# Optimization experiments

Measured on AMD Instinct MI355X. Metric: run time of the kernel, lower is better.

Reference implementation:

```python
import jax, jax.numpy as jnp
import numpy as np

B, S, D, H, L, NITEMS = 512, 200, 64, 2, 2, 100000
HD = D // H
EPS = 1e-8
C = 0.001


def _ln(x, w, b):
    m = jnp.mean(x, -1, keepdims=True)
    v = jnp.mean((x - m) ** 2, -1, keepdims=True)
    return (x - m) / jnp.sqrt(v + EPS) * w + b


def _frob(x):
    return jnp.sqrt(jnp.sum(x * x))


def setup_inputs() -> dict:
    key = jax.random.key(0)
    ks = jax.random.split(key, 20)
    rn = lambda k, shape, s=0.02: jax.random.normal(k, shape, jnp.float32) * s
    item_emb = rn(ks[0], (NITEMS + 1, D))
    pos_emb = rn(ks[1], (S + 1, D)).at[0].set(0.0)  # padding_idx=0 row
    pred_w = rn(ks[2], (1, D))
    inp = {
        'user_ids': jax.random.randint(ks[3], (B,), 0, NITEMS, dtype=jnp.int32),
        'log_seqs': jax.random.randint(ks[4], (B, S), 0, NITEMS + 1, dtype=jnp.int32),
        'pos_seqs': jax.random.randint(ks[5], (B, S), 0, NITEMS + 1, dtype=jnp.int32),
        'item_emb': item_emb, 'pos_emb': pos_emb, 'pred_w': pred_w,
        'ln_w': jnp.ones((L, D), jnp.float32), 'ln_b': rn(ks[6], (L, D)),
        'qkv_w': rn(ks[7], (L, 3 * D, D)), 'qkv_b': rn(ks[8], (L, 3 * D)),
        'out_w': rn(ks[9], (L, D, D)), 'out_b': rn(ks[10], (L, D)),
        'fc1_w': rn(ks[11], (L, D, D)), 'fc1_b': rn(ks[12], (L, D)),
        'ffln_w': jnp.ones((L, D), jnp.float32), 'ffln_b': rn(ks[13], (L, D)),
        'fc2_w': rn(ks[14], (L, D, D)), 'fc2_b': rn(ks[15], (L, D)),
        'ffln2_w': jnp.ones((L, D), jnp.float32), 'ffln2_b': rn(ks[16], (L, D)),
    }
    return inp


def reference(user_ids, log_seqs, pos_seqs, item_emb, pos_emb, pred_w,
              ln_w, ln_b, qkv_w, qkv_b, out_w, out_b,
              fc1_w, fc1_b, ffln_w, ffln_b, fc2_w, fc2_b, ffln2_w, ffln2_b):
    # ---- log2feats ----
    x = item_emb[log_seqs] * jnp.sqrt(jnp.float32(D))  # (B,S,D)
    poss = jnp.arange(1, S + 1, dtype=log_seqs.dtype)[None, :] * (log_seqs != 0)
    x = x + pos_emb[poss]
    causal_bias = jnp.where(jnp.tril(jnp.ones((S, S), bool)), 0.0, -1e30).astype(jnp.float32)
    for l in range(L):
        q_in = _ln(x, ln_w[l], ln_b[l])  # query uses pre-LN, K/V use raw seqs
        q = (q_in @ qkv_w[l, :D].T + qkv_b[l, :D]).reshape(B, S, H, HD)
        k = (x @ qkv_w[l, D:2 * D].T + qkv_b[l, D:2 * D]).reshape(B, S, H, HD)
        v = (x @ qkv_w[l, 2 * D:].T + qkv_b[l, 2 * D:]).reshape(B, S, H, HD)
        sc = jnp.einsum('bqhd,bkhd->bhqk', q, k) / jnp.sqrt(jnp.float32(HD)) + causal_bias
        a = jax.nn.softmax(sc, -1)
        ctx = jnp.einsum('bhqk,bkhd->bqhd', a, v).reshape(B, S, D)
        x = q_in + ctx @ out_w[l].T + out_b[l]
        h = jax.nn.relu(_ln(x, ffln_w[l], ffln_b[l]) @ fc1_w[l].T + fc1_b[l])
        x = h @ fc2_w[l].T + fc2_b[l] + _ln(x, ffln2_w[l], ffln2_b[l])
    # ---- left(): quadratic form via Gram matrices (math identical to outer-product sum) ----
    FF = jnp.einsum('bsi,bsj->ij', x, x)          # sum_b F_b^T F_b  (d,d)
    EE = item_emb.T @ item_emb                      # (d,d)
    hh = pred_w.T @ pred_w                          # (d,d)
    left = C * jnp.sum(FF * EE * hh)
    # ---- right() ----
    ps = (x * item_emb[pos_seqs]) @ pred_w[0]       # (B,S), prediction has no bias
    right = jnp.sum((1.0 - C) * ps ** 2 - 2.0 * ps)
    # ---- reg_loss(): sum of per-parameter Frobenius norms ----
    reg = _frob(item_emb) + _frob(pos_emb) + _frob(pred_w)
    for p in (ln_w, ln_b, qkv_w, qkv_b, out_w, out_b, fc1_w, fc1_b,
              ffln_w, ffln_b, fc2_w, fc2_b, ffln2_w, ffln2_b):
        reg = reg + jnp.sum(jax.vmap(_frob)(p))  # per-layer params are separate tensors
    return left + right + 0.1 * reg
```

## Files before the change

### kernel.cpp

```cpp
#include <hip/hip_runtime.h>
#include <math.h>

#define BB 512
#define SS 200
#define DDIM 64
#define HD 32
#define LL 2
#define NROWS (BB * SS)
#define EPS 1e-8f
#define CC 0.001f
#define GRAM_NB 256
#define LSTRIDE 72
#define XS 68
#define QROWS 208

typedef __attribute__((ext_vector_type(8))) short bf16x8;
typedef __attribute__((ext_vector_type(4))) float f32x4;

__device__ unsigned short g_qb[NROWS * DDIM];
__device__ float g_gpart[2 * GRAM_NB * 4096];

__device__ __forceinline__ float wave_sum(float v) {
#pragma unroll
    for (int o = 32; o > 0; o >>= 1) v += __shfl_xor(v, o, 64);
    return v;
}
__device__ __forceinline__ unsigned short f2b(float f) {
    unsigned u = __float_as_uint(f);
    return (unsigned short)((u + 0x7FFFu + ((u >> 16) & 1u)) >> 16);
}

__device__ __forceinline__ bf16x8 frag_raw(const float* Xf, int row, int c0) {
    const float* p = &Xf[row * XS + c0];
    float4 u = *(const float4*)p;
    float4 v = *(const float4*)(p + 4);
    bf16x8 r;
    r[0] = (short)f2b(u.x); r[1] = (short)f2b(u.y); r[2] = (short)f2b(u.z); r[3] = (short)f2b(u.w);
    r[4] = (short)f2b(v.x); r[5] = (short)f2b(v.y); r[6] = (short)f2b(v.z); r[7] = (short)f2b(v.w);
    return r;
}
__device__ __forceinline__ bf16x8 frag_ln(const float* Xf, const float* stats,
                                          const float* vw, const float* vb,
                                          int row, int c0) {
    float m = stats[row * 2], rs = stats[row * 2 + 1];
    const float* p = &Xf[row * XS + c0];
    float4 u = *(const float4*)p;
    float4 v = *(const float4*)(p + 4);
    bf16x8 r;
    r[0] = (short)f2b((u.x - m) * rs * vw[c0 + 0] + vb[c0 + 0]);
    r[1] = (short)f2b((u.y - m) * rs * vw[c0 + 1] + vb[c0 + 1]);
    r[2] = (short)f2b((u.z - m) * rs * vw[c0 + 2] + vb[c0 + 2]);
    r[3] = (short)f2b((u.w - m) * rs * vw[c0 + 3] + vb[c0 + 3]);
    r[4] = (short)f2b((v.x - m) * rs * vw[c0 + 4] + vb[c0 + 4]);
    r[5] = (short)f2b((v.y - m) * rs * vw[c0 + 5] + vb[c0 + 5]);
    r[6] = (short)f2b((v.z - m) * rs * vw[c0 + 6] + vb[c0 + 6]);
    r[7] = (short)f2b((v.w - m) * rs * vw[c0 + 7] + vb[c0 + 7]);
    return r;
}

__device__ __forceinline__ void stage_wf32(const float* __restrict__ G,
                                           unsigned short* __restrict__ L, int t) {
    int r = t >> 4, c4 = (t & 15) * 4;
    float4 f = *(const float4*)&G[r * 64 + c4];
    ushort4 o; o.x = f2b(f.x); o.y = f2b(f.y); o.z = f2b(f.z); o.w = f2b(f.w);
    *(ushort4*)&L[r * LSTRIDE + c4] = o;
}

__global__ __launch_bounds__(1024)
void mega(const int* __restrict__ log_seqs,
          const int* __restrict__ pos_seqs,
          const float* __restrict__ item_emb,
          const float* __restrict__ pos_emb,
          const float* __restrict__ pred_w,
          const float* __restrict__ ln_w,  const float* __restrict__ ln_b,
          const float* __restrict__ qkv_b,
          const float* __restrict__ out_b,
          const float* __restrict__ fc1_b, const float* __restrict__ fc2_b,
          const float* __restrict__ ffln_w, const float* __restrict__ ffln_b,
          const float* __restrict__ ffln2_w, const float* __restrict__ ffln2_b,
          const float* __restrict__ qkv_w, const float* __restrict__ out_w,
          const float* __restrict__ fc1_w, const float* __restrict__ fc2_w,
          unsigned short* __restrict__ xb,
          float* __restrict__ rpart,
          unsigned int* __restrict__ cnt) {
    __shared__ float Xf[200 * XS];
    __shared__ unsigned short Qb[QROWS * 72];
    __shared__ unsigned short Kb[QROWS * 72];
    __shared__ unsigned short Vt[64 * 232];
    __shared__ unsigned short Wb[64 * LSTRIDE];
    __shared__ float stats[200 * 2];
    __shared__ float vecs[13][64];
    __shared__ float redw[16];

    const int t = threadIdx.x, b = blockIdx.x;
    const int w = t >> 6, lane = t & 63, m16 = lane & 15, quad = lane >> 4;
    const f32x4 Z = {0.f, 0.f, 0.f, 0.f};

    if (b == 0 && t == 0) *cnt = 0u;
    if (t < 64) vecs[12][t] = pred_w[t];
    if (t < 512) {
        int r2 = t >> 3, cc = 200 + (t & 7) * 4;
        ushort4 z4; z4.x = z4.y = z4.z = z4.w = 0;
        *(ushort4*)&Vt[r2 * 232 + cc] = z4;
    }
    {
        int rr = t >> 2;
        if (rr < 200) {
            int li = log_seqs[b * SS + rr];
            int poss = li ? (rr + 1) : 0;
            int qd = (t & 3) * 16;
            float4 v[4];
#pragma unroll
            for (int g = 0; g < 4; ++g) {
                float4 e = *(const float4*)&item_emb[(long)li * DDIM + qd + g * 4];
                float4 p = *(const float4*)&pos_emb[(long)poss * DDIM + qd + g * 4];
                v[g].x = e.x * 8.0f + p.x; v[g].y = e.y * 8.0f + p.y;
                v[g].z = e.z * 8.0f + p.z; v[g].w = e.w * 8.0f + p.w;
                *(float4*)&Xf[rr * XS + qd + g * 4] = v[g];
            }
            float s1 = 0.f, s2 = 0.f;
#pragma unroll
            for (int g = 0; g < 4; ++g) {
                s1 += (v[g].x + v[g].y) + (v[g].z + v[g].w);
                s2 += (v[g].x * v[g].x + v[g].y * v[g].y) + (v[g].z * v[g].z + v[g].w * v[g].w);
            }
            s1 += __shfl_xor(s1, 1, 64); s1 += __shfl_xor(s1, 2, 64);
            s2 += __shfl_xor(s2, 1, 64); s2 += __shfl_xor(s2, 2, 64);
            float mean = s1 * (1.f / 64.f);
            float var = s2 * (1.f / 64.f) - mean * mean;
            float rs = rsqrtf(var + EPS);
            if ((t & 3) == 0) { stats[rr * 2] = mean; stats[rr * 2 + 1] = rs; }
        }
    }
    __syncthreads();

    for (int l = 0; l < LL; ++l) {
        if (t < 64) {
            vecs[0][t] = qkv_b[l * 192 + t];
            vecs[1][t] = qkv_b[l * 192 + 64 + t];
            vecs[2][t] = qkv_b[l * 192 + 128 + t];
            vecs[3][t] = ln_w[l * 64 + t];   vecs[4][t] = ln_b[l * 64 + t];
            vecs[5][t] = out_b[l * 64 + t];
            vecs[6][t] = fc1_b[l * 64 + t];  vecs[7][t] = fc2_b[l * 64 + t];
            vecs[8][t] = ffln_w[l * 64 + t]; vecs[9][t] = ffln_b[l * 64 + t];
            vecs[10][t] = ffln2_w[l * 64 + t]; vecs[11][t] = ffln2_b[l * 64 + t];
        }
        stage_wf32(qkv_w + l * 12288, Wb, t);
        __syncthreads();
        if (w < 13) {
            int tb = w * 16;
            int row = tb + m16; if (row > 199) row = 199;
            bf16x8 a0 = frag_ln(Xf, stats, vecs[3], vecs[4], row, quad * 8);
            bf16x8 a1 = frag_ln(Xf, stats, vecs[3], vecs[4], row, 32 + quad * 8);
#pragma unroll
            for (int nt = 0; nt < 4; ++nt) {
                bf16x8 b0 = *(const bf16x8*)&Wb[(nt * 16 + m16) * LSTRIDE + quad * 8];
                bf16x8 b1 = *(const bf16x8*)&Wb[(nt * 16 + m16) * LSTRIDE + 32 + quad * 8];
                f32x4 acc = Z;
                acc = __builtin_amdgcn_mfma_f32_16x16x32_bf16(a0, b0, acc, 0, 0, 0);
                acc = __builtin_amdgcn_mfma_f32_16x16x32_bf16(a1, b1, acc, 0, 0, 0);
                int n = nt * 16 + m16; float bbv = vecs[0][n];
#pragma unroll
                for (int rg = 0; rg < 4; ++rg)
                    Qb[(tb + quad * 4 + rg) * 72 + n] = f2b(acc[rg] + bbv);
            }
        }
        __syncthreads();
        stage_wf32(qkv_w + l * 12288 + 4096, Wb, t);
        __syncthreads();
        if (w < 13) {
            int tb = w * 16;
            int row = tb + m16; if (row > 199) row = 199;
            bf16x8 a0 = frag_raw(Xf, row, quad * 8);
            bf16x8 a1 = frag_raw(Xf, row, 32 + quad * 8);
#pragma unroll
            for (int nt = 0; nt < 4; ++nt) {
                bf16x8 b0 = *(const bf16x8*)&Wb[(nt * 16 + m16) * LSTRIDE + quad * 8];
                bf16x8 b1 = *(const bf16x8*)&Wb[(nt * 16 + m16) * LSTRIDE + 32 + quad * 8];
                f32x4 acc = Z;
                acc = __builtin_amdgcn_mfma_f32_16x16x32_bf16(a0, b0, acc, 0, 0, 0);
                acc = __builtin_amdgcn_mfma_f32_16x16x32_bf16(a1, b1, acc, 0, 0, 0);
                int n = nt * 16 + m16; float bbv = vecs[1][n];
#pragma unroll
                for (int rg = 0; rg < 4; ++rg)
                    Kb[(tb + quad * 4 + rg) * 72 + n] = f2b(acc[rg] + bbv);
            }
        }
        __syncthreads();
        stage_wf32(qkv_w + l * 12288 + 8192, Wb, t);
        __syncthreads();
        if (w < 13) {
            int tb = w * 16;
            int row = tb + m16; if (row > 199) row = 199;
            bf16x8 a0 = frag_raw(Xf, row, quad * 8);
            bf16x8 a1 = frag_raw(Xf, row, 32 + quad * 8);
#pragma unroll
            for (int nt = 0; nt < 4; ++nt) {
                bf16x8 b0 = *(const bf16x8*)&Wb[(nt * 16 + m16) * LSTRIDE + quad * 8];
                bf16x8 b1 = *(const bf16x8*)&Wb[(nt * 16 + m16) * LSTRIDE + 32 + quad * 8];
                f32x4 acc = Z;
                acc = __builtin_amdgcn_mfma_f32_16x16x32_bf16(a0, b0, acc, 0, 0, 0);
                acc = __builtin_amdgcn_mfma_f32_16x16x32_bf16(a1, b1, acc, 0, 0, 0);
                int n = nt * 16 + m16; float bbv = vecs[2][n];
#pragma unroll
                for (int rg = 0; rg < 4; ++rg) {
                    int m = tb + quad * 4 + rg;
                    if (m < 200) Vt[n * 232 + m] = f2b(acc[rg] + bbv);
                }
            }
        }
        __syncthreads();
        {
            const unsigned long long tab0 = 0x01170016FF19FF18ull;
            const unsigned long long tab1 = 0x0513041203150214ull;
            const unsigned long long tab2 = 0x090F080E07110610ull;
            const unsigned long long tab3 = 0xFFFFFFFF0B0D0A0Cull;
            unsigned long long tv = (w & 8) ? ((w & 4) ? tab3 : tab2) : ((w & 4) ? tab1 : tab0);
            unsigned su = (unsigned)((tv >> ((w & 3) * 16)) & 0xFFFFu);
            const float scale = 0.17677669529663687f;
            for (int slot = 0; slot < 2; ++slot) {
                int u = (su >> (slot * 8)) & 0xFF;
                if (u == 0xFF) break;
                int h = u & 1, qt = u >> 1;
                int q0 = qt * 16;
                int qrow = q0 + m16; if (qrow > 199) qrow = 199;
                bf16x8 qa = *(const bf16x8*)&Qb[qrow * 72 + h * 32 + quad * 8];
                __builtin_amdgcn_wave_barrier();
                unsigned short* ps = &Qb[q0 * 72 + h * 32];
                f32x4 o0 = Z, o1 = Z;
                float lsum[4] = {0.f, 0.f, 0.f, 0.f};
                int np = (qt + 2) >> 1;
                for (int pi = 0; pi < np; ++pi) {
                    int p0 = pi * 32;
                    int kr0 = p0 + m16;      int kr0c = kr0 > 199 ? 199 : kr0;
                    int kr1 = p0 + 16 + m16; int kr1c = kr1 > 199 ? 199 : kr1;
                    bf16x8 kb0 = *(const bf16x8*)&Kb[kr0c * 72 + h * 32 + quad * 8];
                    bf16x8 kb1 = *(const bf16x8*)&Kb[kr1c * 72 + h * 32 + quad * 8];
                    f32x4 s0 = __builtin_amdgcn_mfma_f32_16x16x32_bf16(qa, kb0, Z, 0, 0, 0);
                    f32x4 s1 = __builtin_amdgcn_mfma_f32_16x16x32_bf16(qa, kb1, Z, 0, 0, 0);
                    __builtin_amdgcn_wave_barrier();
#pragma unroll
                    for (int rg = 0; rg < 4; ++rg) {
                        int rglob = q0 + quad * 4 + rg;
                        float e0 = (kr0 <= rglob && kr0 < SS) ? __expf(s0[rg] * scale) : 0.f;
                        float e1 = (kr1 <= rglob && kr1 < SS) ? __expf(s1[rg] * scale) : 0.f;
                        lsum[rg] += e0 + e1;
                        int prow = quad * 4 + rg;
                        ps[prow * 72 + m16] = f2b(e0);
                        ps[prow * 72 + 16 + m16] = f2b(e1);
                    }
                    __builtin_amdgcn_wave_barrier();
                    bf16x8 pa = *(const bf16x8*)&ps[m16 * 72 + quad * 8];
                    bf16x8 vb0 = *(const bf16x8*)&Vt[(h * 32 + m16) * 232 + p0 + quad * 8];
                    bf16x8 vb1 = *(const bf16x8*)&Vt[(h * 32 + 16 + m16) * 232 + p0 + quad * 8];
                    o0 = __builtin_amdgcn_mfma_f32_16x16x32_bf16(pa, vb0, o0, 0, 0, 0);
                    o1 = __builtin_amdgcn_mfma_f32_16x16x32_bf16(pa, vb1, o1, 0, 0, 0);
                }
#pragma unroll
                for (int rg = 0; rg < 4; ++rg)
#pragma unroll
                    for (int o = 1; o <= 8; o <<= 1) lsum[rg] += __shfl_xor(lsum[rg], o, 64);
                __builtin_amdgcn_wave_barrier();
#pragma unroll
                for (int rg = 0; rg < 4; ++rg) {
                    int rglob = q0 + quad * 4 + rg;
                    if (rglob < SS) {
                        float inv = 1.f / lsum[rg];
                        Qb[rglob * 72 + h * 32 + m16] = f2b(o0[rg] * inv);
                        Qb[rglob * 72 + h * 32 + 16 + m16] = f2b(o1[rg] * inv);
                    }
                }
            }
        }
        __syncthreads();
        stage_wf32(out_w + l * 4096, Wb, t);
        __syncthreads();
        if (w < 13) {
            int tb = w * 16;
            int row = tb + m16; if (row > 199) row = 199;
            bf16x8 a0 = *(const bf16x8*)&Qb[row * 72 + quad * 8];
            bf16x8 a1 = *(const bf16x8*)&Qb[row * 72 + 32 + quad * 8];
#pragma unroll
            for (int nt = 0; nt < 4; ++nt) {
                bf16x8 b0 = *(const bf16x8*)&Wb[(nt * 16 + m16) * LSTRIDE + quad * 8];
                bf16x8 b1 = *(const bf16x8*)&Wb[(nt * 16 + m16) * LSTRIDE + 32 + quad * 8];
                f32x4 acc = Z;
                acc = __builtin_amdgcn_mfma_f32_16x16x32_bf16(a0, b0, acc, 0, 0, 0);
                acc = __builtin_amdgcn_mfma_f32_16x16x32_bf16(a1, b1, acc, 0, 0, 0);
                int n = nt * 16 + m16;
                float bbv = vecs[5][n], lw = vecs[3][n], lb = vecs[4][n];
#pragma unroll
                for (int rg = 0; rg < 4; ++rg) {
                    int m = tb + quad * 4 + rg; int mc = m > 199 ? 199 : m;
                    float qin = (Xf[mc * XS + n] - stats[mc * 2]) * stats[mc * 2 + 1] * lw + lb;
                    float x1v = acc[rg] + bbv + qin;
                    if (m < 200) Xf[m * XS + n] = x1v;
                }
            }
            __builtin_amdgcn_wave_barrier();
#pragma unroll
            for (int rg = 0; rg < 4; ++rg) {
                int m = tb + quad * 4 + rg; int mc = m > 199 ? 199 : m;
                float v0 = Xf[mc * XS + 0 + m16];
                float v1 = Xf[mc * XS + 16 + m16];
                float v2 = Xf[mc * XS + 32 + m16];
                float v3 = Xf[mc * XS + 48 + m16];
                float s1 = (v0 + v1) + (v2 + v3);
                float s2 = v0 * v0 + v1 * v1 + v2 * v2 + v3 * v3;
#pragma unroll
                for (int o = 1; o <= 8; o <<= 1) { s1 += __shfl_xor(s1, o, 64); s2 += __shfl_xor(s2, o, 64); }
                float mean = s1 * (1.f / 64.f);
                float var = s2 * (1.f / 64.f) - mean * mean;
                float rs = rsqrtf(var + EPS);
                if (m < 200 && m16 == 0) { stats[m * 2] = mean; stats[m * 2 + 1] = rs; }
#pragma unroll
                for (int nt = 0; nt < 4; ++nt) {
                    int n = nt * 16 + m16;
                    float core = (Xf[mc * XS + n] - mean) * rs;
                    Kb[m * 72 + n] = f2b(core * vecs[8][n] + vecs[9][n]);
                }
            }
        }
        __syncthreads();
        stage_wf32(fc1_w + l * 4096, Wb, t);
        __syncthreads();
        if (w < 13) {
            int tb = w * 16;
            bf16x8 a0 = *(const bf16x8*)&Kb[(tb + m16) * 72 + quad * 8];
            bf16x8 a1 = *(const bf16x8*)&Kb[(tb + m16) * 72 + 32 + quad * 8];
            __builtin_amdgcn_wave_barrier();
#pragma unroll
            for (int nt = 0; nt < 4; ++nt) {
                bf16x8 b0 = *(const bf16x8*)&Wb[(nt * 16 + m16) * LSTRIDE + quad * 8];
                bf16x8 b1 = *(const bf16x8*)&Wb[(nt * 16 + m16) * LSTRIDE + 32 + quad * 8];
                f32x4 acc = Z;
                acc = __builtin_amdgcn_mfma_f32_16x16x32_bf16(a0, b0, acc, 0, 0, 0);
                acc = __builtin_amdgcn_mfma_f32_16x16x32_bf16(a1, b1, acc, 0, 0, 0);
                int n = nt * 16 + m16; float bbv = vecs[6][n];
#pragma unroll
                for (int rg = 0; rg < 4; ++rg)
                    Kb[(tb + quad * 4 + rg) * 72 + n] = f2b(fmaxf(acc[rg] + bbv, 0.f));
            }
        }
        __syncthreads();
        stage_wf32(fc2_w + l * 4096, Wb, t);
        __syncthreads();
        if (w < 13) {
            int tb = w * 16;
            bf16x8 a0 = *(const bf16x8*)&Kb[(tb + m16) * 72 + quad * 8];
            bf16x8 a1 = *(const bf16x8*)&Kb[(tb + m16) * 72 + 32 + quad * 8];
#pragma unroll
            for (int nt = 0; nt < 4; ++nt) {
                bf16x8 b0 = *(const bf16x8*)&Wb[(nt * 16 + m16) * LSTRIDE + quad * 8];
                bf16x8 b1 = *(const bf16x8*)&Wb[(nt * 16 + m16) * LSTRIDE + 32 + quad * 8];
                f32x4 acc = Z;
                acc = __builtin_amdgcn_mfma_f32_16x16x32_bf16(a0, b0, acc, 0, 0, 0);
                acc = __builtin_amdgcn_mfma_f32_16x16x32_bf16(a1, b1, acc, 0, 0, 0);
                int n = nt * 16 + m16;
                float bbv = vecs[7][n], lw = vecs[10][n], lb = vecs[11][n];
#pragma unroll
                for (int rg = 0; rg < 4; ++rg) {
                    int m = tb + quad * 4 + rg; int mc = m > 199 ? 199 : m;
                    float x1v = Xf[mc * XS + n];
                    float ln2 = (x1v - stats[mc * 2]) * stats[mc * 2 + 1] * lw + lb;
                    float xnv = acc[rg] + bbv + ln2;
                    if (m < 200) Xf[m * XS + n] = xnv;
                }
            }
            __builtin_amdgcn_wave_barrier();
#pragma unroll
            for (int rg = 0; rg < 4; ++rg) {
                int m = tb + quad * 4 + rg; int mc = m > 199 ? 199 : m;
                float v0 = Xf[mc * XS + 0 + m16];
                float v1 = Xf[mc * XS + 16 + m16];
                float v2 = Xf[mc * XS + 32 + m16];
                float v3 = Xf[mc * XS + 48 + m16];
                float s1 = (v0 + v1) + (v2 + v3);
                float s2 = v0 * v0 + v1 * v1 + v2 * v2 + v3 * v3;
#pragma unroll
                for (int o = 1; o <= 8; o <<= 1) { s1 += __shfl_xor(s1, o, 64); s2 += __shfl_xor(s2, o, 64); }
                float mean = s1 * (1.f / 64.f);
                float var = s2 * (1.f / 64.f) - mean * mean;
                float rs = rsqrtf(var + EPS);
                if (m < 200 && m16 == 0) { stats[m * 2] = mean; stats[m * 2 + 1] = rs; }
            }
        }
        __syncthreads();
    }

    for (int i = t; i < 3200; i += 1024) {
        int r = i >> 4, c4 = (i & 15) * 4;
        float4 f = *(const float4*)&Xf[r * XS + c4];
        ushort4 o; o.x = f2b(f.x); o.y = f2b(f.y); o.z = f2b(f.z); o.w = f2b(f.w);
        *(ushort4*)&xb[((long)b * SS + r) * DDIM + c4] = o;
    }
    float local = 0.f;
    {
        int rr = t >> 2;
        if (rr < 200) {
            int pi = pos_seqs[b * SS + rr];
            int qd = (t & 3) * 16;
            float v = 0.f;
#pragma unroll
            for (int g = 0; g < 4; ++g) {
                float4 xv = *(const float4*)&Xf[rr * XS + qd + g * 4];
                float4 iv = *(const float4*)&item_emb[(long)pi * DDIM + qd + g * 4];
                const float* pwp = &vecs[12][qd + g * 4];
                v += xv.x * iv.x * pwp[0] + xv.y * iv.y * pwp[1]
                   + xv.z * iv.z * pwp[2] + xv.w * iv.w * pwp[3];
            }
            v += __shfl_xor(v, 1, 64); v += __shfl_xor(v, 2, 64);
            if ((t & 3) == 0) local += (1.0f - CC) * v * v - 2.0f * v;
        }
    }
    local = wave_sum(local);
    if (lane == 0) redw[w] = local;
    __syncthreads();
    if (t == 0) {
        float s = 0.f;
#pragma unroll
        for (int i = 0; i < 16; ++i) s += redw[i];
        rpart[b] = s;
    }
}

__global__ __launch_bounds__(256) void gram_kernel(const float* __restrict__ A0, int n0,
                                                   const unsigned short* __restrict__ A1, int n1,
                                                   float* __restrict__ part) {
    __shared__ unsigned short At[64 * LSTRIDE];
    int t = threadIdx.x;
    int second = blockIdx.x >= GRAM_NB;
    int bid = second ? blockIdx.x - GRAM_NB : blockIdx.x;
    int nrows = second ? n1 : n0;
    int w16 = (t >> 6) * 16, lane = t & 63, m16 = lane & 15, quad = lane >> 4;
    int bi = t & 15, bj = t >> 4;
    f32x4 zero = {0.f, 0.f, 0.f, 0.f};
    f32x4 acc[4] = {zero, zero, zero, zero};
    for (long base = (long)bid * 64; base < nrows; base += (long)GRAM_NB * 64) {
        __syncthreads();
        if (!second) {
            float rv[4][4];
#pragma unroll
            for (int e = 0; e < 4; ++e) {
                long gr = base + bj * 4 + e;
                float4 f = make_float4(0.f, 0.f, 0.f, 0.f);
                if (gr < nrows) f = *(const float4*)&A0[gr * DDIM + bi * 4];
                rv[e][0] = f.x; rv[e][1] = f.y; rv[e][2] = f.z; rv[e][3] = f.w;
            }
#pragma unroll
            for (int e = 0; e < 4; ++e) {
                ushort4 o;
                o.x = f2b(rv[0][e]); o.y = f2b(rv[1][e]); o.z = f2b(rv[2][e]); o.w = f2b(rv[3][e]);
                *(ushort4*)&At[(bi * 4 + e) * LSTRIDE + bj * 4] = o;
            }
        } else {
            ushort4 u[4];
#pragma unroll
            for (int e = 0; e < 4; ++e) {
                long gr = base + bj * 4 + e;
                ushort4 uu; uu.x = uu.y = uu.z = uu.w = 0;
                if (gr < nrows) uu = *(const ushort4*)&A1[gr * DDIM + bi * 4];
                u[e] = uu;
            }
#pragma unroll
            for (int e = 0; e < 4; ++e) {
                ushort4 o;
                o.x = ((const unsigned short*)&u[0])[e];
                o.y = ((const unsigned short*)&u[1])[e];
                o.z = ((const unsigned short*)&u[2])[e];
                o.w = ((const unsigned short*)&u[3])[e];
                *(ushort4*)&At[(bi * 4 + e) * LSTRIDE + bj * 4] = o;
            }
        }
        __syncthreads();
#pragma unroll
        for (int ks = 0; ks < 2; ++ks) {
            bf16x8 a = *(const bf16x8*)&At[(w16 + m16) * LSTRIDE + ks * 32 + quad * 8];
#pragma unroll
            for (int nt = 0; nt < 4; ++nt) {
                bf16x8 bfr = *(const bf16x8*)&At[(nt * 16 + m16) * LSTRIDE + ks * 32 + quad * 8];
                acc[nt] = __builtin_amdgcn_mfma_f32_16x16x32_bf16(a, bfr, acc[nt], 0, 0, 0);
            }
        }
    }
    float* slab = part + (long)blockIdx.x * 4096;
#pragma unroll
    for (int nt = 0; nt < 4; ++nt) {
        int n = nt * 16 + m16;
#pragma unroll
        for (int rg = 0; rg < 4; ++rg) {
            int m = w16 + quad * 4 + rg;
            slab[m * 64 + n] = acc[nt][rg];
        }
    }
}

struct NormEntry { const float* p; int n; };
struct NormArgs { NormEntry e[30]; };

__global__ __launch_bounds__(256) void reduce_final(const float* __restrict__ part,
                                                    float* __restrict__ EE, float* __restrict__ FF,
                                                    NormArgs args, float* __restrict__ norms,
                                                    const float* __restrict__ pred_w,
                                                    const float* __restrict__ rpart,
                                                    unsigned int* __restrict__ cnt,
                                                    float* __restrict__ out) {
    __shared__ float red[256];
    __shared__ float redT[256];
    __shared__ float redR[256];
    __shared__ float p_s[64];
    __shared__ unsigned int amlast;
    int blk = blockIdx.x, t = threadIdx.x;
    if (blk < 32) {
        int which = blk >> 4;
        int p = (blk & 15) * 256 + t;
        const float* basep = part + (long)which * GRAM_NB * 4096;
        float s = 0.f;
        for (int b = 0; b < GRAM_NB; ++b) s += basep[(long)b * 4096 + p];
        (which ? FF : EE)[p] = s;
    } else {
        NormEntry en = args.e[blk - 32];
        float s = 0.f;
        for (int i = t; i < en.n; i += 256) { float v = en.p[i]; s += v * v; }
        red[t] = s;
        for (int o = 128; o > 0; o >>= 1) {
            __syncthreads();
            if (t < o) red[t] += red[t + o];
        }
        __syncthreads();
        if (t == 0) norms[blk - 32] = red[0];
    }
    __threadfence();
    __syncthreads();
    if (t == 0) amlast = atomicAdd(cnt, 1u);
    __syncthreads();
    if (amlast != 61) return;
    __threadfence();
    if (t < 64) p_s[t] = pred_w[t];
    __syncthreads();
    float lf = 0.f, tr = 0.f, rs = 0.f;
    for (int p = t; p < 4096; p += 256) {
        int i = p >> 6, j = p & 63;
        float ee = EE[p];
        lf += FF[p] * ee * p_s[i] * p_s[j];
        if (i == j) tr += ee;
    }
    for (int i = t; i < 512; i += 256) rs += rpart[i];
    red[t] = lf; redT[t] = tr; redR[t] = rs;
    for (int o = 128; o > 0; o >>= 1) {
        __syncthreads();
        if (t < o) { red[t] += red[t + o]; redT[t] += redT[t + o]; redR[t] += redR[t + o]; }
    }
    __syncthreads();
    if (t == 0) {
        float reg = sqrtf(redT[0]);
        for (int s = 0; s < 30; ++s) reg += sqrtf(norms[s]);
        out[0] = CC * red[0] + redR[0] + 0.1f * reg;
    }
}

struct DevPtrs { float* gpart; unsigned short* qb; };

static DevPtrs fetch_ptrs() {
    DevPtrs p;
    (void)hipGetSymbolAddress((void**)&p.gpart, HIP_SYMBOL(g_gpart));
    (void)hipGetSymbolAddress((void**)&p.qb,    HIP_SYMBOL(g_qb));
    return p;
}

extern "C" void kernel_launch(void* const* d_in, const int* in_sizes, int n_in,
                              void* d_out, int out_size, void* d_ws, size_t ws_size,
                              hipStream_t stream) {
    const int*   log_seqs = (const int*)d_in[1];
    const int*   pos_seqs = (const int*)d_in[2];
    const float* item_emb = (const float*)d_in[3];
    const float* pos_emb  = (const float*)d_in[4];
    const float* pred_w   = (const float*)d_in[5];
    const float* ln_w     = (const float*)d_in[6];
    const float* ln_b     = (const float*)d_in[7];
    const float* qkv_w    = (const float*)d_in[8];
    const float* qkv_b    = (const float*)d_in[9];
    const float* out_w    = (const float*)d_in[10];
    const float* out_b    = (const float*)d_in[11];
    const float* fc1_w    = (const float*)d_in[12];
    const float* fc1_b    = (const float*)d_in[13];
    const float* ffln_w   = (const float*)d_in[14];
    const float* ffln_b   = (const float*)d_in[15];
    const float* fc2_w    = (const float*)d_in[16];
    const float* fc2_b    = (const float*)d_in[17];
    const float* ffln2_w  = (const float*)d_in[18];
    const float* ffln2_b  = (const float*)d_in[19];

    static DevPtrs P = fetch_ptrs();

    float* ws    = (float*)d_ws;
    float* rpart = ws;
    unsigned int* cnt = (unsigned int*)(ws + 1600);
    float* nrm   = ws + 1664;
    float* EE    = ws + 2048;
    float* FF    = ws + 6144;

    mega<<<BB, 1024, 0, stream>>>(log_seqs, pos_seqs, item_emb, pos_emb, pred_w,
                                  ln_w, ln_b, qkv_b, out_b, fc1_b, fc2_b,
                                  ffln_w, ffln_b, ffln2_w, ffln2_b,
                                  qkv_w, out_w, fc1_w, fc2_w,
                                  P.qb, rpart, cnt);

    gram_kernel<<<2 * GRAM_NB, 256, 0, stream>>>(item_emb, 100001, P.qb, NROWS, P.gpart);

    NormArgs na;
    int s = 0;
    na.e[s++] = {pos_emb, (SS + 1) * DDIM};
    na.e[s++] = {pred_w, DDIM};
    for (int l = 0; l < LL; ++l) {
        na.e[s++] = {ln_w + l * 64, 64};
        na.e[s++] = {ln_b + l * 64, 64};
        na.e[s++] = {qkv_w + (long)l * 12288, 12288};
        na.e[s++] = {qkv_b + (long)l * 192, 192};
        na.e[s++] = {out_w + (long)l * 4096, 4096};
        na.e[s++] = {out_b + l * 64, 64};
        na.e[s++] = {fc1_w + (long)l * 4096, 4096};
        na.e[s++] = {fc1_b + l * 64, 64};
        na.e[s++] = {ffln_w + l * 64, 64};
        na.e[s++] = {ffln_b + l * 64, 64};
        na.e[s++] = {fc2_w + (long)l * 4096, 4096};
        na.e[s++] = {fc2_b + l * 64, 64};
        na.e[s++] = {ffln2_w + l * 64, 64};
        na.e[s++] = {ffln2_b + l * 64, 64};
    }
    reduce_final<<<62, 256, 0, stream>>>(P.gpart, EE, FF, na, nrm, pred_w, rpart, cnt,
                                         (float*)d_out);
}
```

Before: 240.9 us.

## Pre-convert weights to bf16 once and drop per-stage LDS staging barriers

```diff
diff --git a/kernel.cpp b/kernel.cpp
--- a/kernel.cpp
+++ b/kernel.cpp
@@ -19,6 +19,7 @@
 
 __device__ unsigned short g_qb[NROWS * DDIM];
 __device__ float g_gpart[2 * GRAM_NB * 4096];
+__device__ unsigned short g_wb[49152];
 
 __device__ __forceinline__ float wave_sum(float v) {
 #pragma unroll
@@ -28,6 +29,22 @@
 __device__ __forceinline__ unsigned short f2b(float f) {
     unsigned u = __float_as_uint(f);
     return (unsigned short)((u + 0x7FFFu + ((u >> 16) & 1u)) >> 16);
+}
+
+__global__ __launch_bounds__(256) void prep_weights(const float* __restrict__ qkv_w,
+                                                    const float* __restrict__ out_w,
+                                                    const float* __restrict__ fc1_w,
+                                                    const float* __restrict__ fc2_w,
+                                                    unsigned short* __restrict__ wb) {
+    int i4 = (blockIdx.x * 256 + threadIdx.x) * 4;
+    const float* src; int off;
+    if (i4 < 24576)      { src = qkv_w; off = 0; }
+    else if (i4 < 32768) { src = out_w; off = 24576; }
+    else if (i4 < 40960) { src = fc1_w; off = 32768; }
+    else                 { src = fc2_w; off = 40960; }
+    float4 f = *(const float4*)&src[i4 - off];
+    ushort4 o; o.x = f2b(f.x); o.y = f2b(f.y); o.z = f2b(f.z); o.w = f2b(f.w);
+    *(ushort4*)&wb[i4] = o;
 }
 
 __device__ __forceinline__ bf16x8 frag_raw(const float* Xf, int row, int c0) {
@@ -58,12 +75,15 @@
     return r;
 }
 
-__device__ __forceinline__ void stage_wf32(const float* __restrict__ G,
-                                           unsigned short* __restrict__ L, int t) {
-    int r = t >> 4, c4 = (t & 15) * 4;
-    float4 f = *(const float4*)&G[r * 64 + c4];
-    ushort4 o; o.x = f2b(f.x); o.y = f2b(f.y); o.z = f2b(f.z); o.w = f2b(f.w);
-    *(ushort4*)&L[r * LSTRIDE + c4] = o;
+__device__ __forceinline__ f32x4 gemm1(bf16x8 a0, bf16x8 a1,
+                                       const unsigned short* __restrict__ Wg,
+                                       int nt, int m16, int quad) {
+    bf16x8 b0 = *(const bf16x8*)&Wg[(nt * 16 + m16) * 64 + quad * 8];
+    bf16x8 b1 = *(const bf16x8*)&Wg[(nt * 16 + m16) * 64 + 32 + quad * 8];
+    f32x4 acc = {0.f, 0.f, 0.f, 0.f};
+    acc = __builtin_amdgcn_mfma_f32_16x16x32_bf16(a0, b0, acc, 0, 0, 0);
+    acc = __builtin_amdgcn_mfma_f32_16x16x32_bf16(a1, b1, acc, 0, 0, 0);
+    return acc;
 }
 
 __global__ __launch_bounds__(1024)
@@ -78,8 +98,7 @@
           const float* __restrict__ fc1_b, const float* __restrict__ fc2_b,
           const float* __restrict__ ffln_w, const float* __restrict__ ffln_b,
           const float* __restrict__ ffln2_w, const float* __restrict__ ffln2_b,
-          const float* __restrict__ qkv_w, const float* __restrict__ out_w,
-          const float* __restrict__ fc1_w, const float* __restrict__ fc2_w,
+          const unsigned short* __restrict__ wb,
           unsigned short* __restrict__ xb,
           float* __restrict__ rpart,
           unsigned int* __restrict__ cnt) {
@@ -87,7 +106,6 @@
     __shared__ unsigned short Qb[QROWS * 72];
     __shared__ unsigned short Kb[QROWS * 72];
     __shared__ unsigned short Vt[64 * 232];
-    __shared__ unsigned short Wb[64 * LSTRIDE];
     __shared__ float stats[200 * 2];
     __shared__ float vecs[13][64];
     __shared__ float redw[16];
@@ -132,9 +150,9 @@
             if ((t & 3) == 0) { stats[rr * 2] = mean; stats[rr * 2 + 1] = rs; }
         }
     }
-    __syncthreads();
 
     for (int l = 0; l < LL; ++l) {
+        __syncthreads();
         if (t < 64) {
             vecs[0][t] = qkv_b[l * 192 + t];
             vecs[1][t] = qkv_b[l * 192 + 64 + t];
@@ -145,67 +163,43 @@
             vecs[8][t] = ffln_w[l * 64 + t]; vecs[9][t] = ffln_b[l * 64 + t];
             vecs[10][t] = ffln2_w[l * 64 + t]; vecs[11][t] = ffln2_b[l * 64 + t];
         }
-        stage_wf32(qkv_w + l * 12288, Wb, t);
         __syncthreads();
         if (w < 13) {
+            const unsigned short* wq = wb + l * 12288;
             int tb = w * 16;
             int row = tb + m16; if (row > 199) row = 199;
-            bf16x8 a0 = frag_ln(Xf, stats, vecs[3], vecs[4], row, quad * 8);
-            bf16x8 a1 = frag_ln(Xf, stats, vecs[3], vecs[4], row, 32 + quad * 8);
-#pragma unroll
-            for (int nt = 0; nt < 4; ++nt) {
-                bf16x8 b0 = *(const bf16x8*)&Wb[(nt * 16 + m16) * LSTRIDE + quad * 8];
-                bf16x8 b1 = *(const bf16x8*)&Wb[(nt * 16 + m16) * LSTRIDE + 32 + quad * 8];
-                f32x4 acc = Z;
-                acc = __builtin_amdgcn_mfma_f32_16x16x32_bf16(a0, b0, acc, 0, 0, 0);
-                acc = __builtin_amdgcn_mfma_f32_16x16x32_bf16(a1, b1, acc, 0, 0, 0);
-                int n = nt * 16 + m16; float bbv = vecs[0][n];
-#pragma unroll
-                for (int rg = 0; rg < 4; ++rg)
-                    Qb[(tb + quad * 4 + rg) * 72 + n] = f2b(acc[rg] + bbv);
-            }
-        }
-        __syncthreads();
-        stage_wf32(qkv_w + l * 12288 + 4096, Wb, t);
-        __syncthreads();
-        if (w < 13) {
-            int tb = w * 16;
-            int row = tb + m16; if (row > 199) row = 199;
-            bf16x8 a0 = frag_raw(Xf, row, quad * 8);
-            bf16x8 a1 = frag_raw(Xf, row, 32 + quad * 8);
-#pragma unroll
-            for (int nt = 0; nt < 4; ++nt) {
-                bf16x8 b0 = *(const bf16x8*)&Wb[(nt * 16 + m16) * LSTRIDE + quad * 8];
-                bf16x8 b1 = *(const bf16x8*)&Wb[(nt * 16 + m16) * LSTRIDE + 32 + quad * 8];
-                f32x4 acc = Z;
-                acc = __builtin_amdgcn_mfma_f32_16x16x32_bf16(a0, b0, acc, 0, 0, 0);
-                acc = __builtin_amdgcn_mfma_f32_16x16x32_bf16(a1, b1, acc, 0, 0, 0);
-                int n = nt * 16 + m16; float bbv = vecs[1][n];
-#pragma unroll
-                for (int rg = 0; rg < 4; ++rg)
-                    Kb[(tb + quad * 4 + rg) * 72 + n] = f2b(acc[rg] + bbv);
-            }
-        }
-        __syncthreads();
-        stage_wf32(qkv_w + l * 12288 + 8192, Wb, t);
-        __syncthreads();
-        if (w < 13) {
-            int tb = w * 16;
-            int row = tb + m16; if (row > 199) row = 199;
-            bf16x8 a0 = frag_raw(Xf, row, quad * 8);
-            bf16x8 a1 = frag_raw(Xf, row, 32 + quad * 8);
-#pragma unroll
-            for (int nt = 0; nt < 4; ++nt) {
-                bf16x8 b0 = *(const bf16x8*)&Wb[(nt * 16 + m16) * LSTRIDE + quad * 8];
-                bf16x8 b1 = *(const bf16x8*)&Wb[(nt * 16 + m16) * LSTRIDE + 32 + quad * 8];
-                f32x4 acc = Z;
-                acc = __builtin_amdgcn_mfma_f32_16x16x32_bf16(a0, b0, acc, 0, 0, 0);
-                acc = __builtin_amdgcn_mfma_f32_16x16x32_bf16(a1, b1, acc, 0, 0, 0);
-                int n = nt * 16 + m16; float bbv = vecs[2][n];
-#pragma unroll
-                for (int rg = 0; rg < 4; ++rg) {
-                    int m = tb + quad * 4 + rg;
-                    if (m < 200) Vt[n * 232 + m] = f2b(acc[rg] + bbv);
+            {
+                bf16x8 a0 = frag_ln(Xf, stats, vecs[3], vecs[4], row, quad * 8);
+                bf16x8 a1 = frag_ln(Xf, stats, vecs[3], vecs[4], row, 32 + quad * 8);
+#pragma unroll
+                for (int nt = 0; nt < 4; ++nt) {
+                    f32x4 acc = gemm1(a0, a1, wq, nt, m16, quad);
+                    int n = nt * 16 + m16; float bbv = vecs[0][n];
+#pragma unroll
+                    for (int rg = 0; rg < 4; ++rg)
+                        Qb[(tb + quad * 4 + rg) * 72 + n] = f2b(acc[rg] + bbv);
+                }
+            }
+            {
+                bf16x8 a0 = frag_raw(Xf, row, quad * 8);
+                bf16x8 a1 = frag_raw(Xf, row, 32 + quad * 8);
+#pragma unroll
+                for (int nt = 0; nt < 4; ++nt) {
+                    f32x4 acc = gemm1(a0, a1, wq + 4096, nt, m16, quad);
+                    int n = nt * 16 + m16; float bbv = vecs[1][n];
+#pragma unroll
+                    for (int rg = 0; rg < 4; ++rg)
+                        Kb[(tb + quad * 4 + rg) * 72 + n] = f2b(acc[rg] + bbv);
+                }
+#pragma unroll
+                for (int nt = 0; nt < 4; ++nt) {
+                    f32x4 acc = gemm1(a0, a1, wq + 8192, nt, m16, quad);
+                    int n = nt * 16 + m16; float bbv = vecs[2][n];
+#pragma unroll
+                    for (int rg = 0; rg < 4; ++rg) {
+                        int m = tb + quad * 4 + rg;
+                        if (m < 200) Vt[n * 232 + m] = f2b(acc[rg] + bbv);
+                    }
                 }
             }
         }
@@ -273,120 +267,102 @@
             }
         }
         __syncthreads();
-        stage_wf32(out_w + l * 4096, Wb, t);
-        __syncthreads();
         if (w < 13) {
             int tb = w * 16;
             int row = tb + m16; if (row > 199) row = 199;
-            bf16x8 a0 = *(const bf16x8*)&Qb[row * 72 + quad * 8];
-            bf16x8 a1 = *(const bf16x8*)&Qb[row * 72 + 32 + quad * 8];
-#pragma unroll
-            for (int nt = 0; nt < 4; ++nt) {
-                bf16x8 b0 = *(const bf16x8*)&Wb[(nt * 16 + m16) * LSTRIDE + quad * 8];
-                bf16x8 b1 = *(const bf16x8*)&Wb[(nt * 16 + m16) * LSTRIDE + 32 + quad * 8];
-                f32x4 acc = Z;
-                acc = __builtin_amdgcn_mfma_f32_16x16x32_bf16(a0, b0, acc, 0, 0, 0);
-                acc = __builtin_amdgcn_mfma_f32_16x16x32_bf16(a1, b1, acc, 0, 0, 0);
-                int n = nt * 16 + m16;
-                float bbv = vecs[5][n], lw = vecs[3][n], lb = vecs[4][n];
+            {
+                bf16x8 a0 = *(const bf16x8*)&Qb[row * 72 + quad * 8];
+                bf16x8 a1 = *(const bf16x8*)&Qb[row * 72 + 32 + quad * 8];
+#pragma unroll
+                for (int nt = 0; nt < 4; ++nt) {
+                    f32x4 acc = gemm1(a0, a1, wb + 24576 + l * 4096, nt, m16, quad);
+                    int n = nt * 16 + m16;
+                    float bbv = vecs[5][n], lw = vecs[3][n], lb = vecs[4][n];
+#pragma unroll
+                    for (int rg = 0; rg < 4; ++rg) {
+                        int m = tb + quad * 4 + rg; int mc = m > 199 ? 199 : m;
+                        float qin = (Xf[mc * XS + n] - stats[mc * 2]) * stats[mc * 2 + 1] * lw + lb;
+                        float x1v = acc[rg] + bbv + qin;
+                        if (m < 200) Xf[m * XS + n] = x1v;
+                    }
+                }
+                __builtin_amdgcn_wave_barrier();
 #pragma unroll
                 for (int rg = 0; rg < 4; ++rg) {
                     int m = tb + quad * 4 + rg; int mc = m > 199 ? 199 : m;
-                    float qin = (Xf[mc * XS + n] - stats[mc * 2]) * stats[mc * 2 + 1] * lw + lb;
-                    float x1v = acc[rg] + bbv + qin;
-                    if (m < 200) Xf[m * XS + n] = x1v;
+                    float v0 = Xf[mc * XS + 0 + m16];
+                    float v1 = Xf[mc * XS + 16 + m16];
+                    float v2 = Xf[mc * XS + 32 + m16];
+                    float v3 = Xf[mc * XS + 48 + m16];
+                    float s1 = (v0 + v1) + (v2 + v3);
+                    float s2 = v0 * v0 + v1 * v1 + v2 * v2 + v3 * v3;
+#pragma unroll
+                    for (int o = 1; o <= 8; o <<= 1) { s1 += __shfl_xor(s1, o, 64); s2 += __shfl_xor(s2, o, 64); }
+                    float mean = s1 * (1.f / 64.f);
+                    float var = s2 * (1.f / 64.f) - mean * mean;
+                    float rs = rsqrtf(var + EPS);
+                    if (m < 200 && m16 == 0) { stats[m * 2] = mean; stats[m * 2 + 1] = rs; }
+#pragma unroll
+                    for (int nt = 0; nt < 4; ++nt) {
+                        int n = nt * 16 + m16;
+                        float core = (Xf[mc * XS + n] - mean) * rs;
+                        Kb[m * 72 + n] = f2b(core * vecs[8][n] + vecs[9][n]);
+                    }
                 }
             }
             __builtin_amdgcn_wave_barrier();
-#pragma unroll
-            for (int rg = 0; rg < 4; ++rg) {
-                int m = tb + quad * 4 + rg; int mc = m > 199 ? 199 : m;
-                float v0 = Xf[mc * XS + 0 + m16];
-                float v1 = Xf[mc * XS + 16 + m16];
-                float v2 = Xf[mc * XS + 32 + m16];
-                float v3 = Xf[mc * XS + 48 + m16];
-                float s1 = (v0 + v1) + (v2 + v3);
-                float s2 = v0 * v0 + v1 * v1 + v2 * v2 + v3 * v3;
-#pragma unroll
-                for (int o = 1; o <= 8; o <<= 1) { s1 += __shfl_xor(s1, o, 64); s2 += __shfl_xor(s2, o, 64); }
-                float mean = s1 * (1.f / 64.f);
-                float var = s2 * (1.f / 64.f) - mean * mean;
-                float rs = rsqrtf(var + EPS);
-                if (m < 200 && m16 == 0) { stats[m * 2] = mean; stats[m * 2 + 1] = rs; }
+            {
+                bf16x8 a0 = *(const bf16x8*)&Kb[(tb + m16) * 72 + quad * 8];
+                bf16x8 a1 = *(const bf16x8*)&Kb[(tb + m16) * 72 + 32 + quad * 8];
+                __builtin_amdgcn_wave_barrier();
 #pragma unroll
                 for (int nt = 0; nt < 4; ++nt) {
+                    f32x4 acc = gemm1(a0, a1, wb + 32768 + l * 4096, nt, m16, quad);
+                    int n = nt * 16 + m16; float bbv = vecs[6][n];
+#pragma unroll
+                    for (int rg = 0; rg < 4; ++rg)
+                        Kb[(tb + quad * 4 + rg) * 72 + n] = f2b(fmaxf(acc[rg] + bbv, 0.f));
+                }
+            }
+            __builtin_amdgcn_wave_barrier();
+            {
+                bf16x8 a0 = *(const bf16x8*)&Kb[(tb + m16) * 72 + quad * 8];
+                bf16x8 a1 = *(const bf16x8*)&Kb[(tb + m16) * 72 + 32 + quad * 8];
+#pragma unroll
+                for (int nt = 0; nt < 4; ++nt) {
+                    f32x4 acc = gemm1(a0, a1, wb + 40960 + l * 4096, nt, m16, quad);
                     int n = nt * 16 + m16;
-                    float core = (Xf[mc * XS + n] - mean) * rs;
-                    Kb[m * 72 + n] = f2b(core * vecs[8][n] + vecs[9][n]);
-                }
-            }
-        }
-        __syncthreads();
-        stage_wf32(fc1_w + l * 4096, Wb, t);
-        __syncthreads();
-        if (w < 13) {
-            int tb = w * 16;
-            bf16x8 a0 = *(const bf16x8*)&Kb[(tb + m16) * 72 + quad * 8];
-            bf16x8 a1 = *(const bf16x8*)&Kb[(tb + m16) * 72 + 32 + quad * 8];
-            __builtin_amdgcn_wave_barrier();
-#pragma unroll
-            for (int nt = 0; nt < 4; ++nt) {
-                bf16x8 b0 = *(const bf16x8*)&Wb[(nt * 16 + m16) * LSTRIDE + quad * 8];
-                bf16x8 b1 = *(const bf16x8*)&Wb[(nt * 16 + m16) * LSTRIDE + 32 + quad * 8];
-                f32x4 acc = Z;
-                acc = __builtin_amdgcn_mfma_f32_16x16x32_bf16(a0, b0, acc, 0, 0, 0);
-                acc = __builtin_amdgcn_mfma_f32_16x16x32_bf16(a1, b1, acc, 0, 0, 0);
-                int n = nt * 16 + m16; float bbv = vecs[6][n];
-#pragma unroll
-                for (int rg = 0; rg < 4; ++rg)
-                    Kb[(tb + quad * 4 + rg) * 72 + n] = f2b(fmaxf(acc[rg] + bbv, 0.f));
-            }
-        }
-        __syncthreads();
-        stage_wf32(fc2_w + l * 4096, Wb, t);
-        __syncthreads();
-        if (w < 13) {
-            int tb = w * 16;
-            bf16x8 a0 = *(const bf16x8*)&Kb[(tb + m16) * 72 + quad * 8];
-            bf16x8 a1 = *(const bf16x8*)&Kb[(tb + m16) * 72 + 32 + quad * 8];
-#pragma unroll
-            for (int nt = 0; nt < 4; ++nt) {
-                bf16x8 b0 = *(const bf16x8*)&Wb[(nt * 16 + m16) * LSTRIDE + quad * 8];
-                bf16x8 b1 = *(const bf16x8*)&Wb[(nt * 16 + m16) * LSTRIDE + 32 + quad * 8];
-                f32x4 acc = Z;
-                acc = __builtin_amdgcn_mfma_f32_16x16x32_bf16(a0, b0, acc, 0, 0, 0);
-                acc = __builtin_amdgcn_mfma_f32_16x16x32_bf16(a1, b1, acc, 0, 0, 0);
-                int n = nt * 16 + m16;
-                float bbv = vecs[7][n], lw = vecs[10][n], lb = vecs[11][n];
+                    float bbv = vecs[7][n], lw = vecs[10][n], lb = vecs[11][n];
+#pragma unroll
+                    for (int rg = 0; rg < 4; ++rg) {
+                        int m = tb + quad * 4 + rg; int mc = m > 199 ? 199 : m;
+                        float x1v = Xf[mc * XS + n];
+                        float ln2 = (x1v - stats[mc * 2]) * stats[mc * 2 + 1] * lw + lb;
+                        float xnv = acc[rg] + bbv + ln2;
+                        if (m < 200) Xf[m * XS + n] = xnv;
+                    }
+                }
+                __builtin_amdgcn_wave_barrier();
 #pragma unroll
                 for (int rg = 0; rg < 4; ++rg) {
                     int m = tb + quad * 4 + rg; int mc = m > 199 ? 199 : m;
-                    float x1v = Xf[mc * XS + n];
-                    float ln2 = (x1v - stats[mc * 2]) * stats[mc * 2 + 1] * lw + lb;
-                    float xnv = acc[rg] + bbv + ln2;
-                    if (m < 200) Xf[m * XS + n] = xnv;
-                }
-            }
-            __builtin_amdgcn_wave_barrier();
-#pragma unroll
-            for (int rg = 0; rg < 4; ++rg) {
-                int m = tb + quad * 4 + rg; int mc = m > 199 ? 199 : m;
-                float v0 = Xf[mc * XS + 0 + m16];
-                float v1 = Xf[mc * XS + 16 + m16];
-                float v2 = Xf[mc * XS + 32 + m16];
-                float v3 = Xf[mc * XS + 48 + m16];
-                float s1 = (v0 + v1) + (v2 + v3);
-                float s2 = v0 * v0 + v1 * v1 + v2 * v2 + v3 * v3;
-#pragma unroll
-                for (int o = 1; o <= 8; o <<= 1) { s1 += __shfl_xor(s1, o, 64); s2 += __shfl_xor(s2, o, 64); }
-                float mean = s1 * (1.f / 64.f);
-                float var = s2 * (1.f / 64.f) - mean * mean;
-                float rs = rsqrtf(var + EPS);
-                if (m < 200 && m16 == 0) { stats[m * 2] = mean; stats[m * 2 + 1] = rs; }
-            }
-        }
-        __syncthreads();
-    }
+                    float v0 = Xf[mc * XS + 0 + m16];
+                    float v1 = Xf[mc * XS + 16 + m16];
+                    float v2 = Xf[mc * XS + 32 + m16];
+                    float v3 = Xf[mc * XS + 48 + m16];
+                    float s1 = (v0 + v1) + (v2 + v3);
+                    float s2 = v0 * v0 + v1 * v1 + v2 * v2 + v3 * v3;
+#pragma unroll
+                    for (int o = 1; o <= 8; o <<= 1) { s1 += __shfl_xor(s1, o, 64); s2 += __shfl_xor(s2, o, 64); }
+                    float mean = s1 * (1.f / 64.f);
+                    float var = s2 * (1.f / 64.f) - mean * mean;
+                    float rs = rsqrtf(var + EPS);
+                    if (m < 200 && m16 == 0) { stats[m * 2] = mean; stats[m * 2 + 1] = rs; }
+                }
+            }
+        }
+    }
+    __syncthreads();
 
     for (int i = t; i < 3200; i += 1024) {
         int r = i >> 4, c4 = (i & 15) * 4;
@@ -559,12 +535,13 @@
     }
 }
 
-struct DevPtrs { float* gpart; unsigned short* qb; };
+struct DevPtrs { float* gpart; unsigned short *qb, *wb; };
 
 static DevPtrs fetch_ptrs() {
     DevPtrs p;
     (void)hipGetSymbolAddress((void**)&p.gpart, HIP_SYMBOL(g_gpart));
     (void)hipGetSymbolAddress((void**)&p.qb,    HIP_SYMBOL(g_qb));
+    (void)hipGetSymbolAddress((void**)&p.wb,    HIP_SYMBOL(g_wb));
     return p;
 }
 
@@ -600,11 +577,12 @@
     float* EE    = ws + 2048;
     float* FF    = ws + 6144;
 
+    prep_weights<<<48, 256, 0, stream>>>(qkv_w, out_w, fc1_w, fc2_w, P.wb);
+
     mega<<<BB, 1024, 0, stream>>>(log_seqs, pos_seqs, item_emb, pos_emb, pred_w,
                                   ln_w, ln_b, qkv_b, out_b, fc1_b, fc2_b,
                                   ffln_w, ffln_b, ffln2_w, ffln2_b,
-                                  qkv_w, out_w, fc1_w, fc2_w,
-                                  P.qb, rpart, cnt);
+                                  P.wb, P.qb, rpart, cnt);
 
     gram_kernel<<<2 * GRAM_NB, 256, 0, stream>>>(item_emb, 100001, P.qb, NROWS, P.gpart);
 
```

Result: slower. 268.6 us (+11.5%).
